# Performance work log

Measured on AMD Instinct MI355X. Metric: run time of the kernel, lower is better.

The kernel has to match this reference:

```python
import jax, jax.numpy as jnp
import numpy as np

N_FP = 235336   # n_fingerprint
N_WORD = 7844   # n_word
D = 10          # embed / hidden dim (hard-coded in module)
K = 23          # conv kernel 2*11+1
PAD = 11
N_ATOMS = 4096
L_WORDS = 65536


def setup_inputs() -> dict:
    key = jax.random.key(0)
    ks = jax.random.split(key, 16)
    s = 0.1  # weight init scale
    return {
        "fingerprints": jax.random.randint(ks[0], (N_ATOMS,), 0, N_FP),
        # scale adjacency so x + A@hs stays O(1) over 3 layers
        "adjacency": jax.random.uniform(ks[1], (N_ATOMS, N_ATOMS), dtype=jnp.float32) * (1.0 / N_ATOMS),
        "words": jax.random.randint(ks[2], (L_WORDS,), 0, N_WORD),
        "embed_fp": jax.random.normal(ks[3], (N_FP, D), dtype=jnp.float32) * s,
        "embed_word": jax.random.normal(ks[4], (N_WORD, D), dtype=jnp.float32) * s,
        "W_gnn_w": jax.random.normal(ks[5], (3, D, D), dtype=jnp.float32) * s,
        "W_gnn_b": jax.random.normal(ks[6], (3, D), dtype=jnp.float32) * s,
        "W_cnn_w": jax.random.normal(ks[7], (3, 1, 1, K, K), dtype=jnp.float32) * (s / K),
        "W_cnn_b": jax.random.normal(ks[8], (3,), dtype=jnp.float32) * s,
        "W_att_w": jax.random.normal(ks[9], (D, D), dtype=jnp.float32) * s,
        "W_att_b": jax.random.normal(ks[10], (D,), dtype=jnp.float32) * s,
        "W_out_w": jax.random.normal(ks[11], (3, 2 * D, 2 * D), dtype=jnp.float32) * s,
        "W_out_b": jax.random.normal(ks[12], (3, 2 * D), dtype=jnp.float32) * s,
        "W_int_w": jax.random.normal(ks[13], (2, 2 * D), dtype=jnp.float32) * s,
        "W_int_b": jax.random.normal(ks[14], (2,), dtype=jnp.float32) * s,
    }


def reference(fingerprints, adjacency, words, embed_fp, embed_word,
              W_gnn_w, W_gnn_b, W_cnn_w, W_cnn_b, W_att_w, W_att_b,
              W_out_w, W_out_b, W_int_w, W_int_b):
    # ---- Compound vector with GNN ----
    xs = embed_fp[fingerprints]                       # [N, D]
    for i in range(3):                                # fixed 3 layers
        hs = jax.nn.relu(xs @ W_gnn_w[i].T + W_gnn_b[i])
        xs = xs + adjacency @ hs                      # dense message passing
    compound = jnp.mean(xs, axis=0, keepdims=True)    # [1, D]

    # ---- Protein vector with attention-CNN ----
    ws = embed_word[words]                            # [L, D]
    t = ws[None, None]                                # [1,1,L,D] NCHW
    for i in range(3):
        t = jax.nn.relu(
            jax.lax.conv_general_dilated(t, W_cnn_w[i], (1, 1),
                                          [(PAD, PAD), (PAD, PAD)])
            + W_cnn_b[i])
    xs_p = t[0, 0]                                    # [L, D]

    h = jax.nn.relu(compound @ W_att_w.T + W_att_b)   # [1, D]
    hs_p = jax.nn.relu(xs_p @ W_att_w.T + W_att_b)    # [L, D]
    weights = jnp.tanh(h @ hs_p.T)                    # [1, L]
    ys = weights.T * hs_p                             # [L, D]
    protein = jnp.mean(ys, axis=0, keepdims=True)     # [1, D]

    # ---- Fusion MLP ----
    cat = jnp.concatenate([compound, protein], axis=1)  # [1, 2D]
    for j in range(3):
        cat = jax.nn.relu(cat @ W_out_w[j].T + W_out_b[j])
    return cat @ W_int_w.T + W_int_b                  # [1, 2]
```

## Files before the change

### kernel.cpp

```cpp
#include <hip/hip_runtime.h>
#include <math.h>

#define N_ATOMS 4096
#define L_WORDS 65536
#define DD 10
#define HALO 11

#define CONV_BLOCKS 256
#define CONV_BLOCK 256
#define RPW 8
#define RPB 32
#define QCOLS 1024
#define TOTAL_BLOCKS 768
#define ATT_BLOCKS 64
#define SH_FLOATS 2926

__global__ __launch_bounds__(128) void gnn_embed(
    const int* __restrict__ fp, const float* __restrict__ embed_fp,
    const float* __restrict__ Wg, const float* __restrict__ bg,
    float* __restrict__ xs, float* __restrict__ hs)
{
    const int n = blockIdx.x * 128 + threadIdx.x;
    float x[DD];
    const float* e = embed_fp + (size_t)fp[n] * DD;
    #pragma unroll
    for (int d = 0; d < DD; ++d) x[d] = e[d];
    #pragma unroll
    for (int d = 0; d < DD; ++d) xs[d * N_ATOMS + n] = x[d];
    #pragma unroll
    for (int d = 0; d < DD; ++d) {
        float v = bg[d];
        #pragma unroll
        for (int k = 0; k < DD; ++k) v += Wg[d * DD + k] * x[k];
        hs[d * N_ATOMS + n] = fmaxf(v, 0.f);
    }
}

__global__ __launch_bounds__(128) void gnn_prep(
    const float* __restrict__ xs_in, const float* __restrict__ part,
    const float* __restrict__ Wg, const float* __restrict__ bg,
    float* __restrict__ xs_out, float* __restrict__ hs)
{
    const int n = blockIdx.x * 128 + threadIdx.x;
    float x[DD];
    #pragma unroll
    for (int d = 0; d < DD; ++d) {
        float v = xs_in[d * N_ATOMS + n];
        #pragma unroll
        for (int q = 0; q < 4; ++q)
            v += part[((size_t)q * DD + d) * N_ATOMS + n];
        x[d] = v;
        xs_out[d * N_ATOMS + n] = v;
    }
    #pragma unroll
    for (int d = 0; d < DD; ++d) {
        float v = bg[d];
        #pragma unroll
        for (int k = 0; k < DD; ++k) v += Wg[d * DD + k] * x[k];
        hs[d * N_ATOMS + n] = fmaxf(v, 0.f);
    }
}

__device__ __forceinline__ void conv_stage(
    float* sh, const int tid, const int bx,
    const float* __restrict__ tin, const int* __restrict__ words,
    const float* __restrict__ embed_word, const float* __restrict__ w,
    const float* __restrict__ bptr, float* __restrict__ tout,
    const float* __restrict__ Wa, const float* __restrict__ ba,
    float* __restrict__ hpb)
{
    const int l0 = bx * CONV_BLOCK;
    for (int idx = tid; idx < (CONV_BLOCK + 2 * HALO) * DD; idx += CONV_BLOCK) {
        int rr = idx / DD, d = idx - rr * DD;
        int gr = l0 - HALO + rr;
        float v = 0.f;
        if (gr >= 0 && gr < L_WORDS) {
            if (tin) v = tin[(size_t)gr * DD + d];
            else     v = embed_word[(size_t)words[gr] * DD + d];
        }
        sh[rr * 11 + d] = v;
    }
    __syncthreads();

    const float bias = *bptr;
    float acc[DD];
    #pragma unroll
    for (int d = 0; d < DD; ++d) acc[d] = bias;
    for (int i = 0; i < 23; ++i) {
        float row[DD];
        const float* sr = &sh[(tid + i) * 11];
        #pragma unroll
        for (int c = 0; c < DD; ++c) row[c] = sr[c];
        #pragma unroll
        for (int d = 0; d < DD; ++d) {
            #pragma unroll
            for (int c = 0; c < DD; ++c)
                acc[d] += row[c] * w[i * 23 + (c - d + 11)];
        }
    }
    const int l = l0 + tid;
    if (tout) {
        #pragma unroll
        for (int d = 0; d < DD; ++d)
            tout[(size_t)l * DD + d] = fmaxf(acc[d], 0.f);
    }
    if (hpb) {
        float xsp[DD];
        #pragma unroll
        for (int d = 0; d < DD; ++d) xsp[d] = fmaxf(acc[d], 0.f);
        #pragma unroll
        for (int d = 0; d < DD; ++d) {
            float v = ba[d];
            #pragma unroll
            for (int k = 0; k < DD; ++k) v += Wa[d * DD + k] * xsp[k];
            hpb[(size_t)l * DD + d] = fmaxf(v, 0.f);
        }
    }
}

__device__ __forceinline__ void gnn_stage(
    float* sh, const int tid, const int b,
    const float* __restrict__ hs,
    const float* __restrict__ A, float* __restrict__ part_out)
{
    const int wave = tid >> 6, lane = tid & 63;
    const int q = b & 3, rg = b >> 2;

    const int r0 = rg * RPB + wave * RPW;
    const float4* A4 = (const float4*)(A + (size_t)r0 * N_ATOMS) + q * (QCOLS / 4);
    const float4* h4 = (const float4*)hs + q * (QCOLS / 4);

    float acc[RPW][DD];
    #pragma unroll
    for (int r = 0; r < RPW; ++r)
        #pragma unroll
        for (int d = 0; d < DD; ++d) acc[r][d] = 0.f;

    #pragma unroll 1
    for (int it = 0; it < 4; ++it) {
        const int cb = it * 64 + lane;
        float4 a[RPW];
        #pragma unroll
        for (int r = 0; r < RPW; ++r) a[r] = A4[r * (N_ATOMS / 4) + cb];
        #pragma unroll
        for (int d = 0; d < DD; ++d) {
            float4 h = h4[d * (N_ATOMS / 4) + cb];
            #pragma unroll
            for (int r = 0; r < RPW; ++r) {
                acc[r][d] += a[r].x * h.x;
                acc[r][d] += a[r].y * h.y;
                acc[r][d] += a[r].z * h.z;
                acc[r][d] += a[r].w * h.w;
            }
        }
    }

    #pragma unroll
    for (int m = 1; m <= 4; m <<= 1) {
        #pragma unroll
        for (int r = 0; r < RPW; ++r)
            #pragma unroll
            for (int d = 0; d < DD; ++d)
                acc[r][d] += __shfl_xor(acc[r][d], m, 64);
    }

    if ((lane & 7) == 0) {
        const int g = lane >> 3;
        float* dst = &sh[(wave * 8 + g) * 80];
        #pragma unroll
        for (int r = 0; r < RPW; ++r)
            #pragma unroll
            for (int d = 0; d < DD; ++d) dst[r * DD + d] = acc[r][d];
    }
    __syncthreads();

    float* pdst = part_out + (size_t)q * DD * N_ATOMS + (size_t)rg * RPB;
    for (int o = tid; o < RPB * DD; o += 256) {
        const int d = o >> 5, rr = o & 31;
        const int w8 = rr >> 3, r = rr & 7;
        float v = 0.f;
        #pragma unroll
        for (int g = 0; g < 8; ++g) v += sh[(w8 * 8 + g) * 80 + r * DD + d];
        pdst[d * N_ATOMS + rr] = v;
    }
}

__global__ __launch_bounds__(256, 3) void fused_layer(
    const float* __restrict__ A, const float* __restrict__ hs,
    float* __restrict__ part_out,
    const float* __restrict__ tin, const int* __restrict__ words,
    const float* __restrict__ emb_w, const float* __restrict__ wc,
    const float* __restrict__ bc, float* __restrict__ tout,
    const float* __restrict__ Wa, const float* __restrict__ ba,
    float* __restrict__ hpb)
{
    __shared__ float sh[SH_FLOATS];
    const int tid = threadIdx.x;
    if (blockIdx.x < CONV_BLOCKS)
        conv_stage(sh, tid, blockIdx.x, tin, words, emb_w, wc, bc, tout,
                   Wa, ba, hpb);
    else
        gnn_stage(sh, tid, blockIdx.x - CONV_BLOCKS, hs, A, part_out);
}

__global__ __launch_bounds__(1024) void attn_final(
    const float* __restrict__ xs2, const float* __restrict__ part2,
    const float* __restrict__ hpb,
    const float* __restrict__ Wa, const float* __restrict__ ba,
    const float* __restrict__ Wo, const float* __restrict__ bo,
    const float* __restrict__ Wi, const float* __restrict__ bi,
    float* att_part, unsigned int* ticket, float* __restrict__ out)
{
    __shared__ float red[16][DD];
    __shared__ float shc[DD];
    __shared__ float cat[20];
    __shared__ int islast;
    const int tid = threadIdx.x, wave = tid >> 6, lane = tid & 63;

    float c[DD];
    #pragma unroll
    for (int d = 0; d < DD; ++d) c[d] = 0.f;
    #pragma unroll
    for (int s = 0; s < 4; ++s) {
        const int n = s * 1024 + tid;
        #pragma unroll
        for (int d = 0; d < DD; ++d) {
            float v = xs2[d * N_ATOMS + n];
            #pragma unroll
            for (int qq = 0; qq < 4; ++qq)
                v += part2[((size_t)qq * DD + d) * N_ATOMS + n];
            c[d] += v;
        }
    }
    #pragma unroll
    for (int m = 32; m >= 1; m >>= 1) {
        #pragma unroll
        for (int d = 0; d < DD; ++d) c[d] += __shfl_xor(c[d], m, 64);
    }
    if (lane == 0) {
        #pragma unroll
        for (int d = 0; d < DD; ++d) red[wave][d] = c[d];
    }
    __syncthreads();
    if (tid < DD) {
        float v = 0.f;
        #pragma unroll
        for (int w = 0; w < 16; ++w) v += red[w][tid];
        shc[tid] = v * (1.f / N_ATOMS);
    }
    __syncthreads();

    float h[DD];
    #pragma unroll
    for (int d = 0; d < DD; ++d) {
        float v = ba[d];
        #pragma unroll
        for (int k = 0; k < DD; ++k) v += Wa[d * DD + k] * shc[k];
        h[d] = fmaxf(v, 0.f);
    }
    const int w_ = blockIdx.x * 1024 + tid;
    float hp[DD], dotv = 0.f;
    #pragma unroll
    for (int d = 0; d < DD; ++d) {
        hp[d] = hpb[(size_t)w_ * DD + d];
        dotv += h[d] * hp[d];
    }
    const float wgt = tanhf(dotv);
    float y[DD];
    #pragma unroll
    for (int d = 0; d < DD; ++d) y[d] = wgt * hp[d];
    #pragma unroll
    for (int m = 32; m >= 1; m >>= 1) {
        #pragma unroll
        for (int d = 0; d < DD; ++d) y[d] += __shfl_xor(y[d], m, 64);
    }
    __syncthreads();
    if (lane == 0) {
        #pragma unroll
        for (int d = 0; d < DD; ++d) red[wave][d] = y[d];
    }
    __syncthreads();
    if (tid < DD) {
        float v = 0.f;
        #pragma unroll
        for (int w = 0; w < 16; ++w) v += red[w][tid];
        __hip_atomic_store(att_part + blockIdx.x * DD + tid, v,
                           __ATOMIC_RELAXED, __HIP_MEMORY_SCOPE_AGENT);
    }
    __syncthreads();

    if (tid == 0) {
        unsigned prev = __hip_atomic_fetch_add(ticket, 1u, __ATOMIC_RELAXED,
                                               __HIP_MEMORY_SCOPE_AGENT);
        islast = (prev == ATT_BLOCKS - 1);
    }
    __syncthreads();
    if (!islast) return;
    asm volatile("" ::: "memory");

    float a[DD];
    #pragma unroll
    for (int d = 0; d < DD; ++d) a[d] = 0.f;
    if (tid < ATT_BLOCKS) {
        #pragma unroll
        for (int d = 0; d < DD; ++d)
            a[d] = __hip_atomic_load(att_part + tid * DD + d,
                                     __ATOMIC_RELAXED, __HIP_MEMORY_SCOPE_AGENT);
    }
    if (wave == 0) {
        #pragma unroll
        for (int m = 32; m >= 1; m >>= 1) {
            #pragma unroll
            for (int d = 0; d < DD; ++d) a[d] += __shfl_xor(a[d], m, 64);
        }
    }
    if (tid == 0) {
        #pragma unroll
        for (int d = 0; d < DD; ++d) cat[DD + d] = a[d] * (1.f / L_WORDS);
    }
    if (tid < DD) cat[tid] = shc[tid];
    __syncthreads();
    for (int j = 0; j < 3; ++j) {
        float v = 0.f;
        if (tid < 20) {
            v = bo[j * 20 + tid];
            for (int k = 0; k < 20; ++k) v += Wo[j * 400 + tid * 20 + k] * cat[k];
        }
        __syncthreads();
        if (tid < 20) cat[tid] = fmaxf(v, 0.f);
        __syncthreads();
    }
    if (tid < 2) {
        float v = bi[tid];
        for (int k = 0; k < 20; ++k) v += Wi[tid * 20 + k] * cat[k];
        out[tid] = v;
    }
}

extern "C" void kernel_launch(void* const* d_in, const int* in_sizes, int n_in,
                              void* d_out, int out_size, void* d_ws, size_t ws_size,
                              hipStream_t stream)
{
    const int*   fp     = (const int*)d_in[0];
    const float* A      = (const float*)d_in[1];
    const int*   words  = (const int*)d_in[2];
    const float* emb_fp = (const float*)d_in[3];
    const float* emb_w  = (const float*)d_in[4];
    const float* Wg     = (const float*)d_in[5];
    const float* bg     = (const float*)d_in[6];
    const float* Wc     = (const float*)d_in[7];
    const float* bc     = (const float*)d_in[8];
    const float* Wa     = (const float*)d_in[9];
    const float* ba     = (const float*)d_in[10];
    const float* Wo     = (const float*)d_in[11];
    const float* bo     = (const float*)d_in[12];
    const float* Wi     = (const float*)d_in[13];
    const float* bi     = (const float*)d_in[14];
    float* out = (float*)d_out;
    float* ws  = (float*)d_ws;

    float* xs0   = ws;
    float* xs1   = ws + 40960;
    float* xs2   = ws + 81920;
    float* hs0   = ws + 122880;
    float* hs1   = ws + 163840;
    float* hs2   = ws + 204800;
    float* part0 = ws + 245760;
    float* part1 = ws + 409600;
    float* part2 = ws + 573440;
    float* ta    = ws + 737280;
    float* tb    = ws + 1392640;
    float* hpb   = ta;
    float* att_part = ws + 2048000;
    unsigned int* ticket = (unsigned int*)(ws + 2048640);

    hipMemsetAsync(ticket, 0, sizeof(unsigned int), stream);

    gnn_embed<<<N_ATOMS / 128, 128, 0, stream>>>(fp, emb_fp, Wg, bg, xs0, hs0);

    fused_layer<<<TOTAL_BLOCKS, 256, 0, stream>>>(
        A, hs0, part0,
        nullptr, words, emb_w, Wc, bc, ta, nullptr, nullptr, nullptr);

    gnn_prep<<<N_ATOMS / 128, 128, 0, stream>>>(
        xs0, part0, Wg + 100, bg + 10, xs1, hs1);

    fused_layer<<<TOTAL_BLOCKS, 256, 0, stream>>>(
        A, hs1, part1,
        ta, words, emb_w, Wc + 529, bc + 1, tb, nullptr, nullptr, nullptr);

    gnn_prep<<<N_ATOMS / 128, 128, 0, stream>>>(
        xs1, part1, Wg + 200, bg + 20, xs2, hs2);

    fused_layer<<<TOTAL_BLOCKS, 256, 0, stream>>>(
        A, hs2, part2,
        tb, words, emb_w, Wc + 1058, bc + 2, nullptr, Wa, ba, hpb);

    attn_final<<<ATT_BLOCKS, 1024, 0, stream>>>(
        xs2, part2, hpb, Wa, ba, Wo, bo, Wi, bi, att_part, ticket, out);
}
```

Baseline: 206.3 us.

## Cache bf16 copy of adjacency in first layer and reuse in later GNN layers

The first fused layer converts the fp32 adjacency matrix to bf16 while reading it for the matmul and writes that copy to workspace. The second and third layers then read the half-size bf16 matrix instead of the fp32 one, cutting adjacency traffic in those layers. In exchange the first layer does an extra 32 MB write, and the later layers lose precision because adjacency values are rounded to bf16.

```diff
diff --git a/kernel.cpp b/kernel.cpp
--- a/kernel.cpp
+++ b/kernel.cpp
@@ -15,6 +15,12 @@
 #define ATT_BLOCKS 64
 #define SH_FLOATS 2926
 
+__device__ __forceinline__ unsigned bf16_rne(float f)
+{
+    unsigned u = __float_as_uint(f);
+    return (u + 0x7FFFu + ((u >> 16) & 1u)) >> 16;
+}
+
 __global__ __launch_bounds__(128) void gnn_embed(
     const int* __restrict__ fp, const float* __restrict__ embed_fp,
     const float* __restrict__ Wg, const float* __restrict__ bg,
@@ -118,16 +124,17 @@
     }
 }
 
-__device__ __forceinline__ void gnn_stage(
+__device__ __forceinline__ void gnn_stage0(
     float* sh, const int tid, const int b,
-    const float* __restrict__ hs,
-    const float* __restrict__ A, float* __restrict__ part_out)
+    const float* __restrict__ hs, const float* __restrict__ A,
+    unsigned short* __restrict__ Abf, float* __restrict__ part_out)
 {
     const int wave = tid >> 6, lane = tid & 63;
     const int q = b & 3, rg = b >> 2;
 
     const int r0 = rg * RPB + wave * RPW;
     const float4* A4 = (const float4*)(A + (size_t)r0 * N_ATOMS) + q * (QCOLS / 4);
+    uint2* ab2 = (uint2*)Abf + (size_t)r0 * (N_ATOMS / 4) + q * (QCOLS / 4);
     const float4* h4 = (const float4*)hs + q * (QCOLS / 4);
 
     float acc[RPW][DD];
@@ -142,6 +149,13 @@
         float4 a[RPW];
         #pragma unroll
         for (int r = 0; r < RPW; ++r) a[r] = A4[r * (N_ATOMS / 4) + cb];
+        #pragma unroll
+        for (int r = 0; r < RPW; ++r) {
+            uint2 p;
+            p.x = bf16_rne(a[r].x) | (bf16_rne(a[r].y) << 16);
+            p.y = bf16_rne(a[r].z) | (bf16_rne(a[r].w) << 16);
+            ab2[r * (N_ATOMS / 4) + cb] = p;
+        }
         #pragma unroll
         for (int d = 0; d < DD; ++d) {
             float4 h = h4[d * (N_ATOMS / 4) + cb];
@@ -185,8 +199,96 @@
     }
 }
 
-__global__ __launch_bounds__(256, 3) void fused_layer(
-    const float* __restrict__ A, const float* __restrict__ hs,
+__device__ __forceinline__ void gnn_stageB(
+    float* sh, const int tid, const int b,
+    const float* __restrict__ hs, const unsigned short* __restrict__ Abf,
+    float* __restrict__ part_out)
+{
+    const int wave = tid >> 6, lane = tid & 63;
+    const int q = b & 3, rg = b >> 2;
+
+    const int r0 = rg * RPB + wave * RPW;
+    const uint4* A8 = (const uint4*)(Abf + (size_t)r0 * N_ATOMS) + q * (QCOLS / 8);
+    const float4* h4 = (const float4*)hs + q * (QCOLS / 4);
+
+    float acc[RPW][DD];
+    #pragma unroll
+    for (int r = 0; r < RPW; ++r)
+        #pragma unroll
+        for (int d = 0; d < DD; ++d) acc[r][d] = 0.f;
+
+    #pragma unroll 1
+    for (int it = 0; it < 2; ++it) {
+        uint4 av[RPW];
+        #pragma unroll
+        for (int r = 0; r < RPW; ++r)
+            av[r] = A8[r * (N_ATOMS / 8) + it * 64 + lane];
+        #pragma unroll
+        for (int d = 0; d < DD; ++d) {
+            float4 hA = h4[d * (N_ATOMS / 4) + it * 128 + lane * 2];
+            float4 hB = h4[d * (N_ATOMS / 4) + it * 128 + lane * 2 + 1];
+            #pragma unroll
+            for (int r = 0; r < RPW; ++r) {
+                acc[r][d] += __uint_as_float(av[r].x << 16)          * hA.x;
+                acc[r][d] += __uint_as_float(av[r].x & 0xffff0000u)  * hA.y;
+                acc[r][d] += __uint_as_float(av[r].y << 16)          * hA.z;
+                acc[r][d] += __uint_as_float(av[r].y & 0xffff0000u)  * hA.w;
+                acc[r][d] += __uint_as_float(av[r].z << 16)          * hB.x;
+                acc[r][d] += __uint_as_float(av[r].z & 0xffff0000u)  * hB.y;
+                acc[r][d] += __uint_as_float(av[r].w << 16)          * hB.z;
+                acc[r][d] += __uint_as_float(av[r].w & 0xffff0000u)  * hB.w;
+            }
+        }
+    }
+
+    #pragma unroll
+    for (int m = 1; m <= 4; m <<= 1) {
+        #pragma unroll
+        for (int r = 0; r < RPW; ++r)
+            #pragma unroll
+            for (int d = 0; d < DD; ++d)
+                acc[r][d] += __shfl_xor(acc[r][d], m, 64);
+    }
+
+    if ((lane & 7) == 0) {
+        const int g = lane >> 3;
+        float* dst = &sh[(wave * 8 + g) * 80];
+        #pragma unroll
+        for (int r = 0; r < RPW; ++r)
+            #pragma unroll
+            for (int d = 0; d < DD; ++d) dst[r * DD + d] = acc[r][d];
+    }
+    __syncthreads();
+
+    float* pdst = part_out + (size_t)q * DD * N_ATOMS + (size_t)rg * RPB;
+    for (int o = tid; o < RPB * DD; o += 256) {
+        const int d = o >> 5, rr = o & 31;
+        const int w8 = rr >> 3, r = rr & 7;
+        float v = 0.f;
+        #pragma unroll
+        for (int g = 0; g < 8; ++g) v += sh[(w8 * 8 + g) * 80 + r * DD + d];
+        pdst[d * N_ATOMS + rr] = v;
+    }
+}
+
+__global__ __launch_bounds__(256, 3) void fused_layer0(
+    const float* __restrict__ A, unsigned short* __restrict__ Abf,
+    const float* __restrict__ hs, float* __restrict__ part_out,
+    const int* __restrict__ words, const float* __restrict__ emb_w,
+    const float* __restrict__ wc, const float* __restrict__ bc,
+    float* __restrict__ tout)
+{
+    __shared__ float sh[SH_FLOATS];
+    const int tid = threadIdx.x;
+    if (blockIdx.x < CONV_BLOCKS)
+        conv_stage(sh, tid, blockIdx.x, nullptr, words, emb_w, wc, bc, tout,
+                   nullptr, nullptr, nullptr);
+    else
+        gnn_stage0(sh, tid, blockIdx.x - CONV_BLOCKS, hs, A, Abf, part_out);
+}
+
+__global__ __launch_bounds__(256, 3) void fused_layerB(
+    const unsigned short* __restrict__ Abf, const float* __restrict__ hs,
     float* __restrict__ part_out,
     const float* __restrict__ tin, const int* __restrict__ words,
     const float* __restrict__ emb_w, const float* __restrict__ wc,
@@ -200,7 +302,7 @@
         conv_stage(sh, tid, blockIdx.x, tin, words, emb_w, wc, bc, tout,
                    Wa, ba, hpb);
     else
-        gnn_stage(sh, tid, blockIdx.x - CONV_BLOCKS, hs, A, part_out);
+        gnn_stageB(sh, tid, blockIdx.x - CONV_BLOCKS, hs, Abf, part_out);
 }
 
 __global__ __launch_bounds__(1024) void attn_final(
@@ -373,27 +475,27 @@
     float* hpb   = ta;
     float* att_part = ws + 2048000;
     unsigned int* ticket = (unsigned int*)(ws + 2048640);
+    unsigned short* Abf = (unsigned short*)(ws + 2099200);
 
     hipMemsetAsync(ticket, 0, sizeof(unsigned int), stream);
 
     gnn_embed<<<N_ATOMS / 128, 128, 0, stream>>>(fp, emb_fp, Wg, bg, xs0, hs0);
 
-    fused_layer<<<TOTAL_BLOCKS, 256, 0, stream>>>(
-        A, hs0, part0,
-        nullptr, words, emb_w, Wc, bc, ta, nullptr, nullptr, nullptr);
+    fused_layer0<<<TOTAL_BLOCKS, 256, 0, stream>>>(
+        A, Abf, hs0, part0, words, emb_w, Wc, bc, ta);
 
     gnn_prep<<<N_ATOMS / 128, 128, 0, stream>>>(
         xs0, part0, Wg + 100, bg + 10, xs1, hs1);
 
-    fused_layer<<<TOTAL_BLOCKS, 256, 0, stream>>>(
-        A, hs1, part1,
+    fused_layerB<<<TOTAL_BLOCKS, 256, 0, stream>>>(
+        Abf, hs1, part1,
         ta, words, emb_w, Wc + 529, bc + 1, tb, nullptr, nullptr, nullptr);
 
     gnn_prep<<<N_ATOMS / 128, 128, 0, stream>>>(
         xs1, part1, Wg + 200, bg + 20, xs2, hs2);
 
-    fused_layer<<<TOTAL_BLOCKS, 256, 0, stream>>>(
-        A, hs2, part2,
+    fused_layerB<<<TOTAL_BLOCKS, 256, 0, stream>>>(
+        Abf, hs2, part2,
         tb, words, emb_w, Wc + 1058, bc + 2, nullptr, Wa, ba, hpb);
 
     attn_final<<<ATT_BLOCKS, 1024, 0, stream>>>(
```

Measured after the change: 226.2 us. 1.1x slower.
